# Optimization experiments

Hardware: AMD Instinct MI355X
Metric: run time of the kernel (lower is better)

Reference implementation:

```python
import jax, jax.numpy as jnp
import numpy as np

N_NODES = 100000   # total atoms in the batched graph
N_EDGES = 1600000  # bonds (directed), avg degree 16
N_GRAPHS = 2000    # molecules in the batch
D_IN, D_H, D_OUT = 600, 300, 2  # 600 = embedding_dim(150) * 4


def setup_inputs() -> dict:
    key = jax.random.key(0)
    ks = jax.random.split(key, 8)
    node_feats = jax.random.normal(ks[0], (N_NODES, D_IN), dtype=jnp.float32)
    W1 = jax.random.normal(ks[1], (D_IN, D_H), dtype=jnp.float32) * (1.0 / np.sqrt(D_IN))
    b1 = jnp.zeros((D_H,), dtype=jnp.float32)
    W2 = jax.random.normal(ks[2], (D_H, D_H), dtype=jnp.float32) * (1.0 / np.sqrt(D_H))
    b2 = jnp.zeros((D_H,), dtype=jnp.float32)
    Wfc = jax.random.normal(ks[3], (D_H, D_OUT), dtype=jnp.float32) * (1.0 / np.sqrt(D_H))
    bfc = jnp.zeros((D_OUT,), dtype=jnp.float32)
    src = jax.random.randint(ks[4], (N_EDGES,), 0, N_NODES, dtype=jnp.int32).astype(jnp.int64)
    dst = jax.random.randint(ks[5], (N_EDGES,), 0, N_NODES, dtype=jnp.int32).astype(jnp.int64)
    graph_id = jnp.sort(jax.random.randint(ks[6], (N_NODES,), 0, N_GRAPHS, dtype=jnp.int32)).astype(jnp.int64)
    return {"node_feats": node_feats, "W1": W1, "b1": b1, "W2": W2, "b2": b2,
            "Wfc": Wfc, "bfc": bfc, "src": src, "dst": dst, "graph_id": graph_id}


def _gcn_layer(x, W, b, src, dst, inv_sqrt_out, inv_sqrt_in):
    # DGL GraphConv (norm='both'): h_i = d_i^{-1/2} * sum_{j->i} d_j^{-1/2} (x_j W) + b
    # weight applied before aggregation (in_feats >= out_feats path), math identical either way.
    h = x @ W                                  # [N, d_out]
    m = h * inv_sqrt_out[:, None]              # scale by src out-degree^{-1/2}
    agg = jax.ops.segment_sum(m[src], dst, num_segments=N_NODES)  # [N, d_out]
    return agg * inv_sqrt_in[:, None] + b


def reference(node_feats, W1, b1, W2, b2, Wfc, bfc, src, dst, graph_id):
    ones_e = jnp.ones((src.shape[0],), dtype=node_feats.dtype)
    deg_out = jax.ops.segment_sum(ones_e, src, num_segments=N_NODES)
    deg_in = jax.ops.segment_sum(ones_e, dst, num_segments=N_NODES)
    inv_sqrt_out = jnp.where(deg_out > 0, jax.lax.rsqrt(jnp.maximum(deg_out, 1.0)), 0.0)
    inv_sqrt_in = jnp.where(deg_in > 0, jax.lax.rsqrt(jnp.maximum(deg_in, 1.0)), 0.0)

    h = jax.nn.relu(_gcn_layer(node_feats, W1, b1, src, dst, inv_sqrt_out, inv_sqrt_in))
    h = jax.nn.relu(_gcn_layer(h, W2, b2, src, dst, inv_sqrt_out, inv_sqrt_in))
    p = jax.nn.softmax(h @ Wfc + bfc, axis=-1)  # [N, 2] per-node class probs

    # per-graph mean pooling (unbatch + mean over each graph's nodes)
    pooled_sum = jax.ops.segment_sum(p, graph_id, num_segments=N_GRAPHS)
    counts = jax.ops.segment_sum(jnp.ones((N_NODES,), dtype=p.dtype), graph_id, num_segments=N_GRAPHS)
    return pooled_sum / jnp.maximum(counts, 1.0)[:, None]  # [G, 2]
```

## Files before the change

kernel.cpp:

```cpp
#include <hip/hip_runtime.h>
#include <hip/hip_bf16.h>
#include <hip/hip_fp8.h>

#define N_NODES 100000
#define N_EDGES 1600000
#define N_GRAPHS 2000
#define D_IN 600
#define D_H 300
#define D_OUT 2

#define NPAD 320
#define K1PAD 640
#define K2PAD 320
#define MPAD 100096

typedef __bf16 bf16;
typedef __bf16 bf16x8 __attribute__((ext_vector_type(8)));
typedef float f32x4 __attribute__((ext_vector_type(4)));
typedef float f32x2 __attribute__((ext_vector_type(2)));

__device__ __forceinline__ unsigned char ff8(float f) {
    __hip_fp8_e4m3 t(f); return (unsigned char)t.__x;
}

__global__ __launch_bounds__(256) void count_deg(const int* __restrict__ src,
                                                 const int* __restrict__ dst,
                                                 int* __restrict__ deg_out,
                                                 int* __restrict__ deg_in) {
    int e = blockIdx.x * blockDim.x + threadIdx.x;
    if (e < N_EDGES) {
        atomicAdd(&deg_out[src[e]], 1);
        atomicAdd(&deg_in[dst[e]], 1);
    }
}

__global__ __launch_bounds__(256) void block_sum(const int* __restrict__ deg_in,
                                                 int* __restrict__ bsum) {
    __shared__ int s[256];
    int i = blockIdx.x * 256 + threadIdx.x;
    s[threadIdx.x] = (i < N_NODES) ? deg_in[i] : 0;
    __syncthreads();
    for (int off = 128; off; off >>= 1) {
        if (threadIdx.x < off) s[threadIdx.x] += s[threadIdx.x + off];
        __syncthreads();
    }
    if (threadIdx.x == 0) bsum[blockIdx.x] = s[0];
}

__global__ void scan_serial(const int* __restrict__ bsum, int* __restrict__ boff, int nb) {
    if (threadIdx.x == 0 && blockIdx.x == 0) {
        int run = 0;
        for (int i = 0; i < nb; ++i) { boff[i] = run; run += bsum[i]; }
    }
}

__global__ __launch_bounds__(256) void node_offsets(const int* __restrict__ deg_in,
                                                    const int* __restrict__ deg_out,
                                                    const int* __restrict__ boff,
                                                    int* __restrict__ row_start,
                                                    int* __restrict__ cursor,
                                                    float* __restrict__ inv_in,
                                                    float* __restrict__ inv_out) {
    __shared__ int s[256];
    int i = blockIdx.x * 256 + threadIdx.x;
    int d = (i < N_NODES) ? deg_in[i] : 0;
    s[threadIdx.x] = d;
    __syncthreads();
    for (int off = 1; off < 256; off <<= 1) {
        int v = 0;
        if (threadIdx.x >= off) v = s[threadIdx.x - off];
        __syncthreads();
        if (threadIdx.x >= off) s[threadIdx.x] += v;
        __syncthreads();
    }
    if (i < N_NODES) {
        int excl = s[threadIdx.x] - d;
        int rs = boff[blockIdx.x] + excl;
        row_start[i] = rs;
        cursor[i] = rs;
        int di = deg_in[i];
        int dout = deg_out[i];
        inv_in[i]  = (di   > 0) ? rsqrtf((float)di)   : 0.0f;
        inv_out[i] = (dout > 0) ? rsqrtf((float)dout) : 0.0f;
    }
}

__global__ __launch_bounds__(256) void fill_csr(const int* __restrict__ src,
                                                const int* __restrict__ dst,
                                                int* __restrict__ cursor,
                                                int* __restrict__ adj) {
    int e = blockIdx.x * blockDim.x + threadIdx.x;
    if (e < N_EDGES) {
        int pos = atomicAdd(&cursor[dst[e]], 1);
        adj[pos] = src[e];
    }
}

__global__ __launch_bounds__(256) void conv_bt(const float* __restrict__ W, bf16* __restrict__ Bt,
                                               int K, int N, int Kpad) {
    int idx = blockIdx.x * 256 + threadIdx.x;
    int k = idx % Kpad;
    int n = idx / Kpad;
    if (n >= NPAD) return;
    bf16 v = (bf16)0.0f;
    if (k < K && n < N) v = (bf16)W[(size_t)k * N + n];
    Bt[(size_t)n * Kpad + k] = v;
}

__global__ __launch_bounds__(256) void prep_small(const float* __restrict__ b1,
                                                  const float* __restrict__ b2,
                                                  const float* __restrict__ Wfc,
                                                  float* __restrict__ b1p,
                                                  float* __restrict__ b2p,
                                                  float* __restrict__ wfcp) {
    int i = blockIdx.x * 256 + threadIdx.x;
    if (i < NPAD) {
        b1p[i] = (i < D_H) ? b1[i] : 0.f;
        b2p[i] = (i < D_H) ? b2[i] : 0.f;
    }
    if (i < NPAD * 2) {
        wfcp[i] = (i < D_H * 2) ? Wfc[i] : 0.f;
    }
}

template<int NK, bool AF32>
__global__ __launch_bounds__(512) void gemm_rs(const float* __restrict__ Af,
                                               const bf16* __restrict__ Ab,
                                               const bf16* __restrict__ Bt,
                                               const float* __restrict__ rowscale,
                                               unsigned char* __restrict__ C8,
                                               int M) {
    __shared__ bf16 As[128 * 64];
    __shared__ bf16 Bs[320 * 64];
    const int tid = threadIdx.x;
    const int lane = tid & 63;
    const int wid = tid >> 6;
    const int wr = wid >> 2;
    const int wc = wid & 3;
    const int blockRow = blockIdx.x * 128;
    const int Kpad = NK * 64;
    const size_t rowBytes = (size_t)Kpad * 2;

    f32x4 acc[4][5] = {};

    int aO[2], aRow[2], aKs[2];
    #pragma unroll
    for (int c = 0; c < 2; ++c) {
        int o = c * 8192 + tid * 16;
        int row = o >> 7;
        int slot = (o >> 4) & 7;
        aO[c] = o; aRow[c] = row; aKs[c] = (slot ^ (row & 7)) * 8;
    }
    int bO[5], bRow[5], bKs[5];
    #pragma unroll
    for (int c = 0; c < 5; ++c) {
        int o = c * 8192 + tid * 16;
        int row = o >> 7;
        int slot = (o >> 4) & 7;
        bO[c] = o; bRow[c] = row; bKs[c] = (slot ^ (row & 7)) * 8;
    }

    float4 fA[2][2];
    bf16x8 sA[2];
    bf16x8 sB[5];

    auto loadTile = [&](int t) {
        #pragma unroll
        for (int c = 0; c < 2; ++c) {
            if (AF32) {
                int gr = blockRow + aRow[c];
                int k = t * 64 + aKs[c];
                if (gr < N_NODES && k < D_IN) {
                    const float* p = Af + (size_t)gr * D_IN + k;
                    fA[c][0] = *(const float4*)p;
                    fA[c][1] = *(const float4*)(p + 4);
                } else {
                    fA[c][0] = make_float4(0.f, 0.f, 0.f, 0.f);
                    fA[c][1] = make_float4(0.f, 0.f, 0.f, 0.f);
                }
            } else {
                const char* g = (const char*)Ab + (size_t)(blockRow + aRow[c]) * rowBytes
                                + (size_t)t * 128 + aKs[c] * 2;
                sA[c] = *(const bf16x8*)g;
            }
        }
        #pragma unroll
        for (int c = 0; c < 5; ++c) {
            const char* g = (const char*)Bt + (size_t)bRow[c] * rowBytes
                            + (size_t)t * 128 + bKs[c] * 2;
            sB[c] = *(const bf16x8*)g;
        }
    };

    loadTile(0);

    for (int t = 0; t < NK; ++t) {
        __syncthreads();
        #pragma unroll
        for (int c = 0; c < 2; ++c) {
            bf16x8 v;
            if (AF32) {
                v[0] = (bf16)fA[c][0].x; v[1] = (bf16)fA[c][0].y;
                v[2] = (bf16)fA[c][0].z; v[3] = (bf16)fA[c][0].w;
                v[4] = (bf16)fA[c][1].x; v[5] = (bf16)fA[c][1].y;
                v[6] = (bf16)fA[c][1].z; v[7] = (bf16)fA[c][1].w;
            } else {
                v = sA[c];
            }
            *(bf16x8*)((char*)As + aO[c]) = v;
        }
        #pragma unroll
        for (int c = 0; c < 5; ++c)
            *(bf16x8*)((char*)Bs + bO[c]) = sB[c];
        __syncthreads();
        if (t + 1 < NK) loadTile(t + 1);
        #pragma unroll
        for (int kk = 0; kk < 2; ++kk) {
            int slot = kk * 4 + (lane >> 4);
            bf16x8 af[4], bfr[5];
            #pragma unroll
            for (int mi = 0; mi < 4; ++mi) {
                int row = wr * 64 + mi * 16 + (lane & 15);
                int addr = row * 128 + ((slot ^ (row & 7)) << 4);
                af[mi] = *(const bf16x8*)((const char*)As + addr);
            }
            #pragma unroll
            for (int ni = 0; ni < 5; ++ni) {
                int row = wc * 80 + ni * 16 + (lane & 15);
                int addr = row * 128 + ((slot ^ (row & 7)) << 4);
                bfr[ni] = *(const bf16x8*)((const char*)Bs + addr);
            }
            #pragma unroll
            for (int mi = 0; mi < 4; ++mi)
                #pragma unroll
                for (int ni = 0; ni < 5; ++ni)
                    acc[mi][ni] = __builtin_amdgcn_mfma_f32_16x16x32_bf16(af[mi], bfr[ni], acc[mi][ni], 0, 0, 0);
        }
    }
    #pragma unroll
    for (int mi = 0; mi < 4; ++mi) {
        #pragma unroll
        for (int i = 0; i < 4; ++i) {
            int gr = blockRow + wr * 64 + mi * 16 + ((lane >> 4) << 2) + i;
            if (gr >= M) continue;
            float sc = rowscale[gr];
            #pragma unroll
            for (int ni = 0; ni < 5; ++ni) {
                int gc = wc * 80 + ni * 16 + (lane & 15);
                C8[(size_t)gr * NPAD + gc] = ff8(acc[mi][ni][i] * sc);
            }
        }
    }
}

__device__ __forceinline__ void gather_fp8(const unsigned char* __restrict__ m8,
                                           const int* __restrict__ adj,
                                           int s, int d, int lane, float acc[5]) {
    const int cb = lane * 4;
    const int c4 = 256 + lane;
    int e = 0;
    for (; e + 8 <= d; e += 8) {
        unsigned int u[8], b[8];
        #pragma unroll
        for (int j = 0; j < 8; ++j) {
            const unsigned char* r = m8 + (size_t)adj[s + e + j] * NPAD;
            u[j] = *(const unsigned int*)(r + cb);
            b[j] = r[c4];
        }
        #pragma unroll
        for (int j = 0; j < 8; ++j) {
            f32x2 lo = __builtin_amdgcn_cvt_pk_f32_fp8(u[j], false);
            f32x2 hi = __builtin_amdgcn_cvt_pk_f32_fp8(u[j], true);
            acc[0] += lo[0]; acc[1] += lo[1]; acc[2] += hi[0]; acc[3] += hi[1];
            acc[4] += __builtin_amdgcn_cvt_f32_fp8(b[j], 0);
        }
    }
    if (e + 4 <= d) {
        unsigned int u[4], b[4];
        #pragma unroll
        for (int j = 0; j < 4; ++j) {
            const unsigned char* r = m8 + (size_t)adj[s + e + j] * NPAD;
            u[j] = *(const unsigned int*)(r + cb);
            b[j] = r[c4];
        }
        #pragma unroll
        for (int j = 0; j < 4; ++j) {
            f32x2 lo = __builtin_amdgcn_cvt_pk_f32_fp8(u[j], false);
            f32x2 hi = __builtin_amdgcn_cvt_pk_f32_fp8(u[j], true);
            acc[0] += lo[0]; acc[1] += lo[1]; acc[2] += hi[0]; acc[3] += hi[1];
            acc[4] += __builtin_amdgcn_cvt_f32_fp8(b[j], 0);
        }
        e += 4;
    }
    for (; e < d; ++e) {
        const unsigned char* r = m8 + (size_t)adj[s + e] * NPAD;
        unsigned int u = *(const unsigned int*)(r + cb);
        unsigned int b = r[c4];
        f32x2 lo = __builtin_amdgcn_cvt_pk_f32_fp8(u, false);
        f32x2 hi = __builtin_amdgcn_cvt_pk_f32_fp8(u, true);
        acc[0] += lo[0]; acc[1] += lo[1]; acc[2] += hi[0]; acc[3] += hi[1];
        acc[4] += __builtin_amdgcn_cvt_f32_fp8(b, 0);
    }
}

__global__ __launch_bounds__(256) void aggregate_fp8(const unsigned char* __restrict__ m8,
                                                     const int* __restrict__ row_start,
                                                     const int* __restrict__ deg_in,
                                                     const int* __restrict__ adj,
                                                     const float* __restrict__ inv_in,
                                                     const float* __restrict__ biasp,
                                                     bf16* __restrict__ h) {
    int node = (int)((blockIdx.x * (size_t)blockDim.x + threadIdx.x) >> 6);
    int lane = threadIdx.x & 63;
    if (node >= N_NODES) return;
    int s = row_start[node];
    int d = deg_in[node];
    float acc[5] = {};
    gather_fp8(m8, adj, s, d, lane, acc);
    float sc = inv_in[node];
    int cA = lane * 4;
    int c4 = 256 + lane;
    float4 bq = *(const float4*)(biasp + cA);
    bf16* out = h + (size_t)node * NPAD;
    __bf16 o4[4];
    o4[0] = (bf16)fmaxf(acc[0] * sc + bq.x, 0.f);
    o4[1] = (bf16)fmaxf(acc[1] * sc + bq.y, 0.f);
    o4[2] = (bf16)fmaxf(acc[2] * sc + bq.z, 0.f);
    o4[3] = (bf16)fmaxf(acc[3] * sc + bq.w, 0.f);
    *(float2*)(out + cA) = *(float2*)o4;
    out[c4] = (bf16)fmaxf(acc[4] * sc + biasp[c4], 0.f);
}

__global__ __launch_bounds__(256) void agg2_fc_pool(const unsigned char* __restrict__ m8,
                                                    const int* __restrict__ row_start,
                                                    const int* __restrict__ deg_in,
                                                    const int* __restrict__ adj,
                                                    const float* __restrict__ inv_in,
                                                    const float* __restrict__ biasp,
                                                    const float* __restrict__ wfcp,
                                                    const float* __restrict__ bfc,
                                                    const int* __restrict__ gid,
                                                    float* __restrict__ pooled,
                                                    int* __restrict__ gcount) {
    int node = (int)((blockIdx.x * (size_t)blockDim.x + threadIdx.x) >> 6);
    int lane = threadIdx.x & 63;
    if (node >= N_NODES) return;
    int s = row_start[node];
    int d = deg_in[node];
    float acc[5] = {};
    gather_fp8(m8, adj, s, d, lane, acc);
    float sc = inv_in[node];
    int cA = lane * 4;
    int c4 = 256 + lane;
    float4 bq = *(const float4*)(biasp + cA);
    float h0 = fmaxf(acc[0] * sc + bq.x, 0.f);
    float h1 = fmaxf(acc[1] * sc + bq.y, 0.f);
    float h2 = fmaxf(acc[2] * sc + bq.z, 0.f);
    float h3 = fmaxf(acc[3] * sc + bq.w, 0.f);
    float h4 = fmaxf(acc[4] * sc + biasp[c4], 0.f);
    float4 wA0 = *(const float4*)(wfcp + cA * 2);
    float4 wA1 = *(const float4*)(wfcp + cA * 2 + 4);
    float z0 = h0 * wA0.x + h1 * wA0.z + h2 * wA1.x + h3 * wA1.z;
    float z1 = h0 * wA0.y + h1 * wA0.w + h2 * wA1.y + h3 * wA1.w;
    z0 += h4 * wfcp[c4 * 2];
    z1 += h4 * wfcp[c4 * 2 + 1];
    for (int off = 32; off; off >>= 1) {
        z0 += __shfl_down(z0, off);
        z1 += __shfl_down(z1, off);
    }
    if (lane == 0) {
        float s0 = z0 + bfc[0], s1 = z1 + bfc[1];
        float mx = fmaxf(s0, s1);
        float e0 = __expf(s0 - mx), e1 = __expf(s1 - mx);
        float inv = 1.f / (e0 + e1);
        int g = gid[node];
        atomicAdd(&pooled[g * 2 + 0], e0 * inv);
        atomicAdd(&pooled[g * 2 + 1], e1 * inv);
        atomicAdd(&gcount[g], 1);
    }
}

__global__ __launch_bounds__(256) void finalize(const float* __restrict__ pooled,
                                                const int* __restrict__ gcount,
                                                float* __restrict__ out) {
    int i = blockIdx.x * blockDim.x + threadIdx.x;
    if (i < N_GRAPHS * 2) {
        int g = i >> 1;
        float c = (float)max(gcount[g], 1);
        out[i] = pooled[i] / c;
    }
}

extern "C" void kernel_launch(void* const* d_in, const int* in_sizes, int n_in,
                              void* d_out, int out_size, void* d_ws, size_t ws_size,
                              hipStream_t stream) {
    const float* x   = (const float*)d_in[0];
    const float* W1  = (const float*)d_in[1];
    const float* b1  = (const float*)d_in[2];
    const float* W2  = (const float*)d_in[3];
    const float* b2  = (const float*)d_in[4];
    const float* Wfc = (const float*)d_in[5];
    const float* bfc = (const float*)d_in[6];
    const int* src   = (const int*)d_in[7];
    const int* dst   = (const int*)d_in[8];
    const int* gid   = (const int*)d_in[9];

    char* ws = (char*)d_ws;
    size_t off = 0;
    auto alloc = [&](size_t bytes) -> void* {
        void* p = ws + off;
        off = (off + bytes + 255) & ~(size_t)255;
        return p;
    };
    bf16* h_bf            = (bf16*)alloc((size_t)MPAD * NPAD * 2);
    unsigned char* m8     = (unsigned char*)alloc((size_t)N_NODES * NPAD);
    bf16* B1t    = (bf16*)alloc((size_t)NPAD * K1PAD * 2);
    bf16* B2t    = (bf16*)alloc((size_t)NPAD * K2PAD * 2);
    int*   adj      = (int*)alloc((size_t)N_EDGES * 4);
    int*   row_st   = (int*)alloc((size_t)N_NODES * 4);
    int*   cursor   = (int*)alloc((size_t)N_NODES * 4);
    int*   deg_in   = (int*)alloc((size_t)N_NODES * 4);
    int*   deg_out  = (int*)alloc((size_t)N_NODES * 4);
    float* inv_in   = (float*)alloc((size_t)N_NODES * 4);
    float* inv_out  = (float*)alloc((size_t)N_NODES * 4);
    const int NB = (N_NODES + 255) / 256;
    int*   bsum     = (int*)alloc((size_t)NB * 4);
    int*   boff     = (int*)alloc((size_t)NB * 4);
    float* pooled   = (float*)alloc((size_t)N_GRAPHS * 2 * 4);
    int*   gcount   = (int*)alloc((size_t)N_GRAPHS * 4);
    float* b1p      = (float*)alloc((size_t)NPAD * 4);
    float* b2p      = (float*)alloc((size_t)NPAD * 4);
    float* wfcp     = (float*)alloc((size_t)NPAD * 2 * 4);

    hipMemsetAsync(deg_in, 0, (size_t)N_NODES * 4, stream);
    hipMemsetAsync(deg_out, 0, (size_t)N_NODES * 4, stream);
    hipMemsetAsync(pooled, 0, (size_t)N_GRAPHS * 2 * 4, stream);
    hipMemsetAsync(gcount, 0, (size_t)N_GRAPHS * 4, stream);

    count_deg<<<(N_EDGES + 255) / 256, 256, 0, stream>>>(src, dst, deg_out, deg_in);
    block_sum<<<NB, 256, 0, stream>>>(deg_in, bsum);
    scan_serial<<<1, 64, 0, stream>>>(bsum, boff, NB);
    node_offsets<<<NB, 256, 0, stream>>>(deg_in, deg_out, boff, row_st, cursor, inv_in, inv_out);
    fill_csr<<<(N_EDGES + 255) / 256, 256, 0, stream>>>(src, dst, cursor, adj);

    conv_bt<<<(NPAD * K1PAD + 255) / 256, 256, 0, stream>>>(W1, B1t, D_IN, D_H, K1PAD);
    conv_bt<<<(NPAD * K2PAD + 255) / 256, 256, 0, stream>>>(W2, B2t, D_H, D_H, K2PAD);
    prep_small<<<3, 256, 0, stream>>>(b1, b2, Wfc, b1p, b2p, wfcp);

    gemm_rs<10, true><<<MPAD / 128, 512, 0, stream>>>(x, nullptr, B1t, inv_out, m8, N_NODES);
    aggregate_fp8<<<(N_NODES * 64 + 255) / 256, 256, 0, stream>>>(m8, row_st, deg_in, adj, inv_in, b1p, h_bf);
    gemm_rs<5, false><<<MPAD / 128, 512, 0, stream>>>(nullptr, h_bf, B2t, inv_out, m8, N_NODES);
    agg2_fc_pool<<<(N_NODES * 64 + 255) / 256, 256, 0, stream>>>(m8, row_st, deg_in, adj, inv_in, b2p,
                                                                 wfcp, bfc, gid, pooled, gcount);
    finalize<<<(N_GRAPHS * 2 + 255) / 256, 256, 0, stream>>>(pooled, gcount, (float*)d_out);
}
```

Baseline: 664.9 us.

## Shard fp8 messages into column planes and gather per shard with edge-parallel lanes

Measured after the change: 1.130 ms. +69.9%, slower.

```diff
diff --git a/kernel.cpp b/kernel.cpp
--- a/kernel.cpp
+++ b/kernel.cpp
@@ -13,8 +13,10 @@
 #define K1PAD 640
 #define K2PAD 320
 #define MPAD 100096
+#define PLANE 4000000
 
 typedef __bf16 bf16;
+typedef __bf16 bf16x4 __attribute__((ext_vector_type(4)));
 typedef __bf16 bf16x8 __attribute__((ext_vector_type(8)));
 typedef float f32x4 __attribute__((ext_vector_type(4)));
 typedef float f32x2 __attribute__((ext_vector_type(2)));
@@ -247,137 +249,122 @@
             #pragma unroll
             for (int ni = 0; ni < 5; ++ni) {
                 int gc = wc * 80 + ni * 16 + (lane & 15);
-                C8[(size_t)gr * NPAD + gc] = ff8(acc[mi][ni][i] * sc);
-            }
-        }
-    }
-}
-
-__device__ __forceinline__ void gather_fp8(const unsigned char* __restrict__ m8,
-                                           const int* __restrict__ adj,
-                                           int s, int d, int lane, float acc[5]) {
-    const int cb = lane * 4;
-    const int c4 = 256 + lane;
-    int e = 0;
-    for (; e + 8 <= d; e += 8) {
-        unsigned int u[8], b[8];
-        #pragma unroll
-        for (int j = 0; j < 8; ++j) {
-            const unsigned char* r = m8 + (size_t)adj[s + e + j] * NPAD;
-            u[j] = *(const unsigned int*)(r + cb);
-            b[j] = r[c4];
-        }
-        #pragma unroll
-        for (int j = 0; j < 8; ++j) {
-            f32x2 lo = __builtin_amdgcn_cvt_pk_f32_fp8(u[j], false);
-            f32x2 hi = __builtin_amdgcn_cvt_pk_f32_fp8(u[j], true);
+                int g = gc / 40;
+                int o = gc - g * 40;
+                C8[(size_t)g * PLANE + (size_t)gr * 40 + o] = ff8(acc[mi][ni][i] * sc);
+            }
+        }
+    }
+}
+
+template<bool FUSE_FC>
+__global__ __launch_bounds__(256) void agg_shard(const unsigned char* __restrict__ m8,
+                                                 const int* __restrict__ row_start,
+                                                 const int* __restrict__ deg_in,
+                                                 const int* __restrict__ adj,
+                                                 const float* __restrict__ inv_in,
+                                                 const float* __restrict__ biasp,
+                                                 const float* __restrict__ wfcp,
+                                                 bf16* __restrict__ h,
+                                                 float2* __restrict__ zpart) {
+    __shared__ f32x4 red[256];
+    const int lane = threadIdx.x & 63;
+    const int wid = threadIdx.x >> 6;
+    const int g = blockIdx.x & 7;
+    const int node = (blockIdx.x >> 3) * 4 + wid;
+    const int s = __builtin_nontemporal_load(row_start + node);
+    const int d = __builtin_nontemporal_load(deg_in + node);
+    const int eslot = lane / 10;
+    const int di = lane - eslot * 10;
+    const bool active = lane < 60;
+    const unsigned char* plane = m8 + (size_t)g * PLANE;
+    const int di4 = di * 4;
+
+    int adjv = (lane < d) ? __builtin_nontemporal_load(adj + s + lane) : 0;
+
+    f32x4 acc = {0.f, 0.f, 0.f, 0.f};
+    for (int e = 0; e < d; e += 18) {
+        unsigned int u[3] = {0u, 0u, 0u};
+        #pragma unroll
+        for (int q = 0; q < 3; ++q) {
+            int ee = e + q * 6 + eslot;
+            bool v = active && (ee < d);
+            int idx = __builtin_amdgcn_ds_bpermute(ee << 2, adjv);
+            if (ee >= 64 && v) idx = __builtin_nontemporal_load(adj + s + ee);
+            if (v) u[q] = *(const unsigned int*)(plane + (size_t)idx * 40 + di4);
+        }
+        #pragma unroll
+        for (int q = 0; q < 3; ++q) {
+            f32x2 lo = __builtin_amdgcn_cvt_pk_f32_fp8(u[q], false);
+            f32x2 hi = __builtin_amdgcn_cvt_pk_f32_fp8(u[q], true);
             acc[0] += lo[0]; acc[1] += lo[1]; acc[2] += hi[0]; acc[3] += hi[1];
-            acc[4] += __builtin_amdgcn_cvt_f32_fp8(b[j], 0);
-        }
-    }
-    if (e + 4 <= d) {
-        unsigned int u[4], b[4];
-        #pragma unroll
-        for (int j = 0; j < 4; ++j) {
-            const unsigned char* r = m8 + (size_t)adj[s + e + j] * NPAD;
-            u[j] = *(const unsigned int*)(r + cb);
-            b[j] = r[c4];
-        }
-        #pragma unroll
-        for (int j = 0; j < 4; ++j) {
-            f32x2 lo = __builtin_amdgcn_cvt_pk_f32_fp8(u[j], false);
-            f32x2 hi = __builtin_amdgcn_cvt_pk_f32_fp8(u[j], true);
-            acc[0] += lo[0]; acc[1] += lo[1]; acc[2] += hi[0]; acc[3] += hi[1];
-            acc[4] += __builtin_amdgcn_cvt_f32_fp8(b[j], 0);
-        }
-        e += 4;
-    }
-    for (; e < d; ++e) {
-        const unsigned char* r = m8 + (size_t)adj[s + e] * NPAD;
-        unsigned int u = *(const unsigned int*)(r + cb);
-        unsigned int b = r[c4];
-        f32x2 lo = __builtin_amdgcn_cvt_pk_f32_fp8(u, false);
-        f32x2 hi = __builtin_amdgcn_cvt_pk_f32_fp8(u, true);
-        acc[0] += lo[0]; acc[1] += lo[1]; acc[2] += hi[0]; acc[3] += hi[1];
-        acc[4] += __builtin_amdgcn_cvt_f32_fp8(b, 0);
-    }
-}
-
-__global__ __launch_bounds__(256) void aggregate_fp8(const unsigned char* __restrict__ m8,
-                                                     const int* __restrict__ row_start,
-                                                     const int* __restrict__ deg_in,
-                                                     const int* __restrict__ adj,
-                                                     const float* __restrict__ inv_in,
-                                                     const float* __restrict__ biasp,
-                                                     bf16* __restrict__ h) {
-    int node = (int)((blockIdx.x * (size_t)blockDim.x + threadIdx.x) >> 6);
-    int lane = threadIdx.x & 63;
-    if (node >= N_NODES) return;
-    int s = row_start[node];
-    int d = deg_in[node];
-    float acc[5] = {};
-    gather_fp8(m8, adj, s, d, lane, acc);
-    float sc = inv_in[node];
-    int cA = lane * 4;
-    int c4 = 256 + lane;
-    float4 bq = *(const float4*)(biasp + cA);
-    bf16* out = h + (size_t)node * NPAD;
-    __bf16 o4[4];
-    o4[0] = (bf16)fmaxf(acc[0] * sc + bq.x, 0.f);
-    o4[1] = (bf16)fmaxf(acc[1] * sc + bq.y, 0.f);
-    o4[2] = (bf16)fmaxf(acc[2] * sc + bq.z, 0.f);
-    o4[3] = (bf16)fmaxf(acc[3] * sc + bq.w, 0.f);
-    *(float2*)(out + cA) = *(float2*)o4;
-    out[c4] = (bf16)fmaxf(acc[4] * sc + biasp[c4], 0.f);
-}
-
-__global__ __launch_bounds__(256) void agg2_fc_pool(const unsigned char* __restrict__ m8,
-                                                    const int* __restrict__ row_start,
-                                                    const int* __restrict__ deg_in,
-                                                    const int* __restrict__ adj,
-                                                    const float* __restrict__ inv_in,
-                                                    const float* __restrict__ biasp,
-                                                    const float* __restrict__ wfcp,
-                                                    const float* __restrict__ bfc,
-                                                    const int* __restrict__ gid,
-                                                    float* __restrict__ pooled,
-                                                    int* __restrict__ gcount) {
-    int node = (int)((blockIdx.x * (size_t)blockDim.x + threadIdx.x) >> 6);
-    int lane = threadIdx.x & 63;
-    if (node >= N_NODES) return;
-    int s = row_start[node];
-    int d = deg_in[node];
-    float acc[5] = {};
-    gather_fp8(m8, adj, s, d, lane, acc);
-    float sc = inv_in[node];
-    int cA = lane * 4;
-    int c4 = 256 + lane;
-    float4 bq = *(const float4*)(biasp + cA);
-    float h0 = fmaxf(acc[0] * sc + bq.x, 0.f);
-    float h1 = fmaxf(acc[1] * sc + bq.y, 0.f);
-    float h2 = fmaxf(acc[2] * sc + bq.z, 0.f);
-    float h3 = fmaxf(acc[3] * sc + bq.w, 0.f);
-    float h4 = fmaxf(acc[4] * sc + biasp[c4], 0.f);
-    float4 wA0 = *(const float4*)(wfcp + cA * 2);
-    float4 wA1 = *(const float4*)(wfcp + cA * 2 + 4);
-    float z0 = h0 * wA0.x + h1 * wA0.z + h2 * wA1.x + h3 * wA1.z;
-    float z1 = h0 * wA0.y + h1 * wA0.w + h2 * wA1.y + h3 * wA1.w;
-    z0 += h4 * wfcp[c4 * 2];
-    z1 += h4 * wfcp[c4 * 2 + 1];
-    for (int off = 32; off; off >>= 1) {
-        z0 += __shfl_down(z0, off);
-        z1 += __shfl_down(z1, off);
-    }
-    if (lane == 0) {
-        float s0 = z0 + bfc[0], s1 = z1 + bfc[1];
-        float mx = fmaxf(s0, s1);
-        float e0 = __expf(s0 - mx), e1 = __expf(s1 - mx);
-        float inv = 1.f / (e0 + e1);
-        int g = gid[node];
-        atomicAdd(&pooled[g * 2 + 0], e0 * inv);
-        atomicAdd(&pooled[g * 2 + 1], e1 * inv);
-        atomicAdd(&gcount[g], 1);
-    }
+        }
+    }
+    red[threadIdx.x] = acc;
+    __syncthreads();
+    if (lane < 10) {
+        f32x4 a = red[wid * 64 + lane];
+        #pragma unroll
+        for (int k = 1; k < 6; ++k) {
+            f32x4 b = red[wid * 64 + k * 10 + lane];
+            a[0] += b[0]; a[1] += b[1]; a[2] += b[2]; a[3] += b[3];
+        }
+        float sc = __builtin_nontemporal_load(inv_in + node);
+        int c = g * 40 + lane * 4;
+        float4 bq = *(const float4*)(biasp + c);
+        float h0 = fmaxf(a[0] * sc + bq.x, 0.f);
+        float h1 = fmaxf(a[1] * sc + bq.y, 0.f);
+        float h2 = fmaxf(a[2] * sc + bq.z, 0.f);
+        float h3 = fmaxf(a[3] * sc + bq.w, 0.f);
+        if (!FUSE_FC) {
+            bf16x4 o;
+            o[0] = (bf16)h0; o[1] = (bf16)h1; o[2] = (bf16)h2; o[3] = (bf16)h3;
+            unsigned long long bits;
+            __builtin_memcpy(&bits, &o, 8);
+            __builtin_nontemporal_store(bits, (unsigned long long*)(h + (size_t)node * NPAD + c));
+        } else {
+            float4 w0 = *(const float4*)(wfcp + c * 2);
+            float4 w1 = *(const float4*)(wfcp + c * 2 + 4);
+            float z0 = h0 * w0.x + h1 * w0.z + h2 * w1.x + h3 * w1.z;
+            float z1 = h0 * w0.y + h1 * w0.w + h2 * w1.y + h3 * w1.w;
+            red[wid * 64 + lane] = f32x4{z0, z1, 0.f, 0.f};
+        }
+    }
+    if (FUSE_FC) {
+        __syncthreads();
+        if (lane == 0) {
+            float z0 = 0.f, z1 = 0.f;
+            #pragma unroll
+            for (int k = 0; k < 10; ++k) {
+                f32x4 v = red[wid * 64 + k];
+                z0 += v[0]; z1 += v[1];
+            }
+            f32x2 zp = {z0, z1};
+            unsigned long long bits;
+            __builtin_memcpy(&bits, &zp, 8);
+            __builtin_nontemporal_store(bits, (unsigned long long*)(zpart + (size_t)node * 8 + g));
+        }
+    }
+}
+
+__global__ __launch_bounds__(256) void pool_final(const float4* __restrict__ zp4,
+                                                  const float* __restrict__ bfc,
+                                                  const int* __restrict__ gid,
+                                                  float* __restrict__ pooled,
+                                                  int* __restrict__ gcount) {
+    int n = blockIdx.x * 256 + threadIdx.x;
+    if (n >= N_NODES) return;
+    const float4* p = zp4 + (size_t)n * 4;
+    float4 a = p[0], b = p[1], c = p[2], d = p[3];
+    float z0 = (a.x + a.z) + (b.x + b.z) + (c.x + c.z) + (d.x + d.z) + bfc[0];
+    float z1 = (a.y + a.w) + (b.y + b.w) + (c.y + c.w) + (d.y + d.w) + bfc[1];
+    float mx = fmaxf(z0, z1);
+    float e0 = __expf(z0 - mx), e1 = __expf(z1 - mx);
+    float inv = 1.f / (e0 + e1);
+    int g = gid[n];
+    atomicAdd(&pooled[g * 2 + 0], e0 * inv);
+    atomicAdd(&pooled[g * 2 + 1], e1 * inv);
+    atomicAdd(&gcount[g], 1);
 }
 
 __global__ __launch_bounds__(256) void finalize(const float* __restrict__ pooled,
@@ -413,7 +400,8 @@
         return p;
     };
     bf16* h_bf            = (bf16*)alloc((size_t)MPAD * NPAD * 2);
-    unsigned char* m8     = (unsigned char*)alloc((size_t)N_NODES * NPAD);
+    unsigned char* m8     = (unsigned char*)alloc((size_t)8 * PLANE);
+    float2* zpart         = (float2*)alloc((size_t)N_NODES * 8 * 8);
     bf16* B1t    = (bf16*)alloc((size_t)NPAD * K1PAD * 2);
     bf16* B2t    = (bf16*)alloc((size_t)NPAD * K2PAD * 2);
     int*   adj      = (int*)alloc((size_t)N_EDGES * 4);
@@ -447,10 +435,14 @@
     conv_bt<<<(NPAD * K2PAD + 255) / 256, 256, 0, stream>>>(W2, B2t, D_H, D_H, K2PAD);
     prep_small<<<3, 256, 0, stream>>>(b1, b2, Wfc, b1p, b2p, wfcp);
 
+    const int AGG_BLOCKS = 8 * (N_NODES / 4);
+
     gemm_rs<10, true><<<MPAD / 128, 512, 0, stream>>>(x, nullptr, B1t, inv_out, m8, N_NODES);
-    aggregate_fp8<<<(N_NODES * 64 + 255) / 256, 256, 0, stream>>>(m8, row_st, deg_in, adj, inv_in, b1p, h_bf);
+    agg_shard<false><<<AGG_BLOCKS, 256, 0, stream>>>(m8, row_st, deg_in, adj, inv_in, b1p,
+                                                     wfcp, h_bf, zpart);
     gemm_rs<5, false><<<MPAD / 128, 512, 0, stream>>>(nullptr, h_bf, B2t, inv_out, m8, N_NODES);
-    agg2_fc_pool<<<(N_NODES * 64 + 255) / 256, 256, 0, stream>>>(m8, row_st, deg_in, adj, inv_in, b2p,
-                                                                 wfcp, bfc, gid, pooled, gcount);
+    agg_shard<true><<<AGG_BLOCKS, 256, 0, stream>>>(m8, row_st, deg_in, adj, inv_in, b2p,
+                                                    wfcp, h_bf, zpart);
+    pool_final<<<(N_NODES + 255) / 256, 256, 0, stream>>>((const float4*)zpart, bfc, gid, pooled, gcount);
     finalize<<<(N_GRAPHS * 2 + 255) / 256, 256, 0, stream>>>(pooled, gcount, (float*)d_out);
 }
```
